# Optimization experiments

Hardware: AMD Instinct MI355X
Metric: run time of the kernel (lower is better)

The kernel has to match this reference:

```python
import jax, jax.numpy as jnp
import numpy as np
from jax import lax

D = 300          # embedding dim (data.x.shape[1])
H = 1024         # hidden_state_dim
H2 = H // 2
V_SENSES = 25000   # last_idx_senses
V_GLOBALS = 50000  # last_idx_globals - last_idx_senses
NUM_NODES = 80000
T = 1024           # seq_len (batch=1)


def _lin_init(k, out_f, in_f):
    # torch.nn.Linear default: U(-1/sqrt(in), 1/sqrt(in)) for W and b
    kw, kb = jax.random.split(k)
    lim = 1.0 / np.sqrt(in_f)
    W = jax.random.uniform(kw, (out_f, in_f), jnp.float32, -lim, lim)
    b = jax.random.uniform(kb, (out_f,), jnp.float32, -lim, lim)
    return W, b


def setup_inputs() -> dict:
    key = jax.random.key(0)
    ks = jax.random.split(key, 6)
    X = jax.random.normal(ks[0], (NUM_NODES, D), jnp.float32) * 0.1
    W1, b1 = _lin_init(ks[1], H, D + H)
    W2, b2 = _lin_init(ks[2], H2, H + H2)
    Wg, bg = _lin_init(ks[3], V_GLOBALS, H2)
    Ws, bs = _lin_init(ks[4], V_SENSES, H2)
    indices = jax.random.randint(ks[5], (1, T), 0, NUM_NODES, jnp.int32)
    return {"X": X, "W1": W1, "b1": b1, "W2": W2, "b2": b2,
            "Wg": Wg, "bg": bg, "Ws": Ws, "bs": bs, "indices": indices}


def reference(X, W1, b1, W2, b2, Wg, bg, Ws, bs, indices):
    # Sequential RNN over flattened (batch, seq) steps; memory_h1/h2 start at
    # zeros and carry across all steps (as the in-place .data.copy_ does).
    # Dropout is treated as identity (eval mode).
    idx = indices.reshape(-1)  # [T]

    def step(carry, i):
        h1, h2 = carry  # [H], [H2]
        e = X[i]  # gather current-word embedding, [D]
        h1n = jax.nn.leaky_relu(
            jnp.dot(W1, jnp.concatenate([e, h1])) + b1, negative_slope=0.01)
        h2n = jax.nn.leaky_relu(
            jnp.dot(W2, jnp.concatenate([h1n, h2])) + b2, negative_slope=0.01)
        return (h1n, h2n), h2n

    init = (jnp.zeros((H,), X.dtype), jnp.zeros((H2,), X.dtype))
    _, h2s = lax.scan(step, init, idx)  # h2s: [T, H2]

    # Output projections batched over all timesteps (same math as per-step).
    logp_globals = jax.nn.log_softmax(h2s @ Wg.T + bg, axis=-1)  # [T, V_GLOBALS]
    logp_senses = jax.nn.log_softmax(h2s @ Ws.T + bs, axis=-1)   # [T, V_SENSES]
    return logp_globals, logp_senses
```

## Files before the change

### kernel.cpp

```cpp
#include <hip/hip_runtime.h>
#include <hip/hip_bf16.h>
#include <stdint.h>

#define T_STEPS 1024
#define NH1 1024
#define NH2 512
#define D_IN 300
#define W1_LD 1324
#define W2_LD 1536
#define NVG 50000
#define NVS 25000

typedef unsigned long long u64;
typedef __bf16 bf16x8 __attribute__((ext_vector_type(8)));
typedef short s16x8 __attribute__((ext_vector_type(8)));
typedef float f32x4 __attribute__((ext_vector_type(4)));

__global__ __launch_bounds__(256) void e_kernel(
    const float* __restrict__ X,
    const float* __restrict__ W1,
    const float* __restrict__ b1,
    const int* __restrict__ idx,
    float* __restrict__ E,
    unsigned* __restrict__ ctl)
{
  if (blockIdx.x == 0 && threadIdx.x < 16) ctl[threadIdx.x] = 0u;

  __shared__ float Xs[32 * 300];
  const int rb = blockIdx.x & 7;
  const int tb = blockIdx.x >> 3;
  const int r0 = rb * 128;
  const int t0 = tb * 32;

  for (int t = 0; t < 32; ++t) {
    int node = idx[t0 + t];
    for (int c = threadIdx.x; c < 300; c += 256)
      Xs[t * 300 + c] = X[(size_t)node * D_IN + c];
  }
  __syncthreads();

  const int rl = threadIdx.x & 127;
  const int th = threadIdx.x >> 7;
  const int tbase = th * 16;
  const int r = r0 + rl;

  float acc[16];
  const float bias = b1[r];
#pragma unroll
  for (int tt = 0; tt < 16; ++tt) acc[tt] = bias;

  const float* wrow = W1 + (size_t)r * W1_LD;
  for (int c0 = 0; c0 < 300; c0 += 4) {
    float w0 = wrow[c0 + 0];
    float w1 = wrow[c0 + 1];
    float w2 = wrow[c0 + 2];
    float w3 = wrow[c0 + 3];
#pragma unroll
    for (int tt = 0; tt < 16; ++tt) {
      const float* xr = Xs + (tbase + tt) * 300 + c0;
      acc[tt] += w0 * xr[0] + w1 * xr[1] + w2 * xr[2] + w3 * xr[3];
    }
  }
#pragma unroll
  for (int tt = 0; tt < 16; ++tt)
    E[(size_t)(t0 + tbase + tt) * NH1 + r] = acc[tt];
}

__global__ __launch_bounds__(256, 2) void rnn_kernel(
    const float* __restrict__ W1,
    const float* __restrict__ W2,
    const float* __restrict__ b2,
    const float* __restrict__ E,
    u64* __restrict__ buf1,
    u64* __restrict__ buf2,
    __hip_bfloat16* __restrict__ h2s,
    unsigned* __restrict__ ctl)
{
  __shared__ float lds1[2][NH1];
  __shared__ float lds2[2][NH2];
  __shared__ int s_role;

  if (threadIdx.x == 0) {
    int xcd;
    asm volatile("s_getreg_b32 %0, hwreg(HW_REG_XCC_ID)" : "=s"(xcd));
    xcd &= 7;
    unsigned rk = atomicAdd(&ctl[xcd], 1u);
    int role = -1;
    if (rk < 64u) {
      if (rk == 63u) atomicCAS(&ctl[8], 0u, (unsigned)(xcd + 1));
      unsigned wnr;
      while ((wnr = __hip_atomic_load(&ctl[8], __ATOMIC_RELAXED,
                                      __HIP_MEMORY_SCOPE_AGENT)) == 0u)
        __builtin_amdgcn_s_sleep(16);
      if (wnr == (unsigned)(xcd + 1)) role = (int)rk;
    }
    s_role = role;
  }
  __syncthreads();
  if (s_role < 0) return;
  const int b = s_role;

  const int lane = threadIdx.x & 63;
  const int w = threadIdx.x >> 6;
  const int wvid = b * 4 + w;
  const int r1 = wvid * 4;
  const int r2 = wvid * 2;
  const int q = (w + b) & 3;

  float w1r[4][16];
#pragma unroll
  for (int i = 0; i < 4; ++i)
#pragma unroll
    for (int j = 0; j < 16; ++j)
      w1r[i][j] = W1[(size_t)(r1 + i) * W1_LD + D_IN + lane + 64 * j];

  float w2r[2][24];
#pragma unroll
  for (int i = 0; i < 2; ++i)
#pragma unroll
    for (int j = 0; j < 24; ++j)
      w2r[i][j] = W2[(size_t)(r2 + i) * W2_LD + lane + 64 * j];

  const float b2a = b2[r2];
  const float b2b = b2[r2 + 1];

  for (int s = 0; s <= T_STEPS; ++s) {
    float ev = 0.f;
    if (s < T_STEPS) ev = E[(size_t)s * NH1 + r1 + (lane & 3)];

    float v1[4] = {0.f, 0.f, 0.f, 0.f};
    float v2[2] = {0.f, 0.f};
    unsigned miss = 0;
    if (s >= 1) miss |= 0xFu;
    if (s >= 2) miss |= 0x30u;
    const u64* p1 = buf1 + (size_t)(s & 3) * NH1 + 256 * q + lane;
    const u64* p2 = buf2 + (size_t)((s - 1) & 3) * NH2 + 128 * q + lane;
    const unsigned tag1 = (unsigned)s;
    const unsigned tag2 = (unsigned)(s - 1);

    while (miss) {
      u64 t1[4], t2[2];
      asm volatile(
          "global_load_dwordx2 %0, %6, off sc0 sc1\n\t"
          "global_load_dwordx2 %1, %6, off offset:512 sc0 sc1\n\t"
          "global_load_dwordx2 %2, %6, off offset:1024 sc0 sc1\n\t"
          "global_load_dwordx2 %3, %6, off offset:1536 sc0 sc1\n\t"
          "global_load_dwordx2 %4, %7, off sc0 sc1\n\t"
          "global_load_dwordx2 %5, %7, off offset:512 sc0 sc1\n\t"
          "s_waitcnt vmcnt(0)"
          : "=&v"(t1[0]), "=&v"(t1[1]), "=&v"(t1[2]), "=&v"(t1[3]),
            "=&v"(t2[0]), "=&v"(t2[1])
          : "v"(p1), "v"(p2)
          : "memory");
#pragma unroll
      for (int j = 0; j < 4; ++j)
        if ((miss & (1u << j)) && (unsigned)(t1[j] >> 32) == tag1) {
          v1[j] = __uint_as_float((unsigned)t1[j]);
          miss &= ~(1u << j);
        }
#pragma unroll
      for (int j = 0; j < 2; ++j)
        if ((miss & (0x10u << j)) && (unsigned)(t2[j] >> 32) == tag2) {
          v2[j] = __uint_as_float((unsigned)t2[j]);
          miss &= ~(0x10u << j);
        }
    }

    const int pb = s & 1;
#pragma unroll
    for (int j = 0; j < 4; ++j) lds1[pb][256 * q + 64 * j + lane] = v1[j];
#pragma unroll
    for (int j = 0; j < 2; ++j) lds2[pb][128 * q + 64 * j + lane] = v2[j];
    __syncthreads();

    float a0 = 0.f, a1 = 0.f, a2 = 0.f, a3 = 0.f, a4 = 0.f, a5 = 0.f;
#pragma unroll
    for (int j = 0; j < 16; ++j) {
      float h = lds1[pb][lane + 64 * j];
      a0 += w1r[0][j] * h;
      a1 += w1r[1][j] * h;
      a2 += w1r[2][j] * h;
      a3 += w1r[3][j] * h;
      a4 += w2r[0][j] * h;
      a5 += w2r[1][j] * h;
    }
#pragma unroll
    for (int j = 0; j < 8; ++j) {
      float h = lds2[pb][lane + 64 * j];
      a4 += w2r[0][16 + j] * h;
      a5 += w2r[1][16 + j] * h;
    }

#pragma unroll
    for (int off = 32; off; off >>= 1) {
      a0 += __shfl_xor(a0, off);
      a1 += __shfl_xor(a1, off);
      a2 += __shfl_xor(a2, off);
      a3 += __shfl_xor(a3, off);
    }
    if (s < T_STEPS && lane < 4) {
      float x = (lane == 0 ? a0 : lane == 1 ? a1 : lane == 2 ? a2 : a3) + ev;
      float h = x > 0.f ? x : 0.01f * x;
      u64 pk = ((u64)(unsigned)(s + 1) << 32) | (u64)__float_as_uint(h);
      u64* dst = buf1 + (size_t)((s + 1) & 3) * NH1 + r1 + lane;
      asm volatile("global_store_dwordx2 %0, %1, off sc0"
                   :: "v"(dst), "v"(pk) : "memory");
    }

    if (s >= 1) {
#pragma unroll
      for (int off = 32; off; off >>= 1) {
        a4 += __shfl_xor(a4, off);
        a5 += __shfl_xor(a5, off);
      }
      if (lane >= 4 && lane < 6) {
        int i = lane - 4;
        float x = (i == 0 ? a4 : a5) + (i == 0 ? b2a : b2b);
        float h = x > 0.f ? x : 0.01f * x;
        u64 pk = ((u64)(unsigned)s << 32) | (u64)__float_as_uint(h);
        u64* dst = buf2 + (size_t)(s & 3) * NH2 + r2 + i;
        asm volatile("global_store_dwordx2 %0, %1, off sc0"
                     :: "v"(dst), "v"(pk) : "memory");
        h2s[(size_t)(s - 1) * NH2 + r2 + i] = __float2bfloat16(h);
      }
    }
  }
}

__global__ __launch_bounds__(256, 1) void gemm_kernel(
    const __hip_bfloat16* __restrict__ A,
    const float* __restrict__ B,
    const float* __restrict__ bias,
    float* __restrict__ C,
    int N)
{
  __shared__ short As[256 * 64];
  __shared__ short Bs[128 * 64];
  const int tid = threadIdx.x;
  const int lane = tid & 63;
  const int wv = tid >> 6;
  const int wm = (wv & 1) * 128;
  const int wn = (wv >> 1) * 64;
  const int m0 = blockIdx.x * 256;
  const int n0 = blockIdx.y * 128;
  const int ml = lane & 15;
  const int kq = lane >> 4;

  f32x4 acc[8][4];
#pragma unroll
  for (int i = 0; i < 8; ++i)
#pragma unroll
    for (int j = 0; j < 4; ++j)
      acc[i][j] = (f32x4){0.f, 0.f, 0.f, 0.f};

  for (int kb = 0; kb < 512; kb += 64) {
    __syncthreads();
#pragma unroll
    for (int q = 0; q < 8; ++q) {
      int ch = q * 256 + tid;
      int row = ch >> 3;
      int kc = ch & 7;
      int phys = kc ^ (row & 7);
      s16x8 av = *(const s16x8*)((const short*)A + (size_t)(m0 + row) * 512 + kb + kc * 8);
      *(s16x8*)(As + row * 64 + phys * 8) = av;
    }
#pragma unroll
    for (int q = 0; q < 4; ++q) {
      int ch = q * 256 + tid;
      int row = ch >> 3;
      int kc = ch & 7;
      int phys = kc ^ (row & 7);
      int gr = n0 + row;
      if (gr >= N) gr = N - 1;
      const float* src = B + (size_t)gr * 512 + kb + kc * 8;
      f32x4 f0 = *(const f32x4*)(src);
      f32x4 f1 = *(const f32x4*)(src + 4);
      bf16x8 bv;
      bv[0] = (__bf16)f0[0]; bv[1] = (__bf16)f0[1];
      bv[2] = (__bf16)f0[2]; bv[3] = (__bf16)f0[3];
      bv[4] = (__bf16)f1[0]; bv[5] = (__bf16)f1[1];
      bv[6] = (__bf16)f1[2]; bv[7] = (__bf16)f1[3];
      *(bf16x8*)(Bs + row * 64 + phys * 8) = bv;
    }
    __syncthreads();
#pragma unroll
    for (int ks = 0; ks < 2; ++ks) {
      bf16x8 af[8], bfr[4];
#pragma unroll
      for (int i = 0; i < 8; ++i) {
        int row = wm + 16 * i + ml;
        int phys = (ks * 4 + kq) ^ (row & 7);
        af[i] = *(const bf16x8*)(As + row * 64 + phys * 8);
      }
#pragma unroll
      for (int j = 0; j < 4; ++j) {
        int row = wn + 16 * j + ml;
        int phys = (ks * 4 + kq) ^ (row & 7);
        bfr[j] = *(const bf16x8*)(Bs + row * 64 + phys * 8);
      }
#pragma unroll
      for (int i = 0; i < 8; ++i)
#pragma unroll
        for (int j = 0; j < 4; ++j)
          acc[i][j] = __builtin_amdgcn_mfma_f32_16x16x32_bf16(af[i], bfr[j], acc[i][j], 0, 0, 0);
    }
  }

  float bv[4];
#pragma unroll
  for (int j = 0; j < 4; ++j) {
    int n = n0 + wn + 16 * j + ml;
    bv[j] = (n < N) ? bias[n] : 0.f;
  }
#pragma unroll
  for (int i = 0; i < 8; ++i) {
    int mrow = m0 + wm + 16 * i + kq * 4;
#pragma unroll
    for (int j = 0; j < 4; ++j) {
      int n = n0 + wn + 16 * j + ml;
      if (n < N) {
#pragma unroll
        for (int r = 0; r < 4; ++r)
          C[(size_t)(mrow + r) * N + n] = acc[i][j][r] + bv[j];
      }
    }
  }
}

__global__ __launch_bounds__(256) void norm_kernel(float* __restrict__ out)
{
  const int b = blockIdx.x;
  const int t = b & 1023;
  const int seg = b >> 10;
  const size_t base = seg == 0 ? (size_t)t * NVG
                               : (size_t)1024 * NVG + (size_t)t * NVS;
  const int len = seg == 0 ? NVG : NVS;
  float* p = out + base;
  const int lane = threadIdx.x & 63;
  const int wv = threadIdx.x >> 6;
  __shared__ float red[4];

  float m = -3.0e38f;
  for (int i = threadIdx.x; i < len; i += 256)
    m = fmaxf(m, p[i]);
#pragma unroll
  for (int off = 32; off; off >>= 1) m = fmaxf(m, __shfl_xor(m, off));
  if (lane == 0) red[wv] = m;
  __syncthreads();
  m = fmaxf(fmaxf(red[0], red[1]), fmaxf(red[2], red[3]));
  __syncthreads();

  float sum = 0.f;
  for (int i = threadIdx.x; i < len; i += 256)
    sum += expf(p[i] - m);
#pragma unroll
  for (int off = 32; off; off >>= 1) sum += __shfl_xor(sum, off);
  if (lane == 0) red[wv] = sum;
  __syncthreads();
  sum = red[0] + red[1] + red[2] + red[3];
  const float lse = m + logf(sum);

  for (int i = threadIdx.x; i < len; i += 256)
    p[i] = p[i] - lse;
}

extern "C" void kernel_launch(void* const* d_in, const int* in_sizes, int n_in,
                              void* d_out, int out_size, void* d_ws, size_t ws_size,
                              hipStream_t stream) {
  const float* X  = (const float*)d_in[0];
  const float* W1 = (const float*)d_in[1];
  const float* b1 = (const float*)d_in[2];
  const float* W2 = (const float*)d_in[3];
  const float* b2 = (const float*)d_in[4];
  const float* Wg = (const float*)d_in[5];
  const float* bg = (const float*)d_in[6];
  const float* Ws = (const float*)d_in[7];
  const float* bs = (const float*)d_in[8];
  const int* idx = (const int*)d_in[9];
  float* out = (float*)d_out;

  char* ws = (char*)d_ws;
  float* E = (float*)ws;
  __hip_bfloat16* h2s = (__hip_bfloat16*)(ws + (size_t)4194304);
  u64* buf1 = (u64*)(ws + (size_t)5242880);
  u64* buf2 = (u64*)(ws + (size_t)5275648);
  unsigned* ctl = (unsigned*)(out + (size_t)1024 * (NVG + NVS) - 16);

  e_kernel<<<256, 256, 0, stream>>>(X, W1, b1, idx, E, ctl);
  rnn_kernel<<<512, 256, 0, stream>>>(W1, W2, b2, E, buf1, buf2, h2s, ctl);
  gemm_kernel<<<dim3(4, 391), 256, 0, stream>>>(h2s, Wg, bg, out, NVG);
  gemm_kernel<<<dim3(4, 196), 256, 0, stream>>>(h2s, Ws, bs,
                                                out + (size_t)1024 * NVG, NVS);
  norm_kernel<<<2048, 256, 0, stream>>>(out);
}
```

Measured before the change: 3.178 ms.

## Split recurrent step into two phases so layer-1 output publishes before waiting on h2

Each step of the persistent RNN kernel used to poll for h1(s) and h2(s-1) together, then compute both layers. It now polls only h1(s), computes and publishes the layer-1 result first, and only then polls h2(s-1) and computes layer 2. The aim is to shorten the critical path of the cross-block layer-1 recurrence, so it no longer waits on the slower h2 flags. In exchange it adds a second __syncthreads and a second polling loop per step, and lds1 is read twice.

```diff
diff --git a/kernel.cpp b/kernel.cpp
--- a/kernel.cpp
+++ b/kernel.cpp
@@ -127,53 +127,37 @@
   for (int s = 0; s <= T_STEPS; ++s) {
     float ev = 0.f;
     if (s < T_STEPS) ev = E[(size_t)s * NH1 + r1 + (lane & 3)];
+    const int pb = s & 1;
 
     float v1[4] = {0.f, 0.f, 0.f, 0.f};
-    float v2[2] = {0.f, 0.f};
-    unsigned miss = 0;
-    if (s >= 1) miss |= 0xFu;
-    if (s >= 2) miss |= 0x30u;
+    unsigned missA = (s >= 1) ? 0xFu : 0u;
     const u64* p1 = buf1 + (size_t)(s & 3) * NH1 + 256 * q + lane;
-    const u64* p2 = buf2 + (size_t)((s - 1) & 3) * NH2 + 128 * q + lane;
     const unsigned tag1 = (unsigned)s;
-    const unsigned tag2 = (unsigned)(s - 1);
-
-    while (miss) {
-      u64 t1[4], t2[2];
+
+    while (missA) {
+      u64 t1[4];
       asm volatile(
-          "global_load_dwordx2 %0, %6, off sc0 sc1\n\t"
-          "global_load_dwordx2 %1, %6, off offset:512 sc0 sc1\n\t"
-          "global_load_dwordx2 %2, %6, off offset:1024 sc0 sc1\n\t"
-          "global_load_dwordx2 %3, %6, off offset:1536 sc0 sc1\n\t"
-          "global_load_dwordx2 %4, %7, off sc0 sc1\n\t"
-          "global_load_dwordx2 %5, %7, off offset:512 sc0 sc1\n\t"
+          "global_load_dwordx2 %0, %4, off sc0 sc1\n\t"
+          "global_load_dwordx2 %1, %4, off offset:512 sc0 sc1\n\t"
+          "global_load_dwordx2 %2, %4, off offset:1024 sc0 sc1\n\t"
+          "global_load_dwordx2 %3, %4, off offset:1536 sc0 sc1\n\t"
           "s_waitcnt vmcnt(0)"
-          : "=&v"(t1[0]), "=&v"(t1[1]), "=&v"(t1[2]), "=&v"(t1[3]),
-            "=&v"(t2[0]), "=&v"(t2[1])
-          : "v"(p1), "v"(p2)
+          : "=&v"(t1[0]), "=&v"(t1[1]), "=&v"(t1[2]), "=&v"(t1[3])
+          : "v"(p1)
           : "memory");
 #pragma unroll
       for (int j = 0; j < 4; ++j)
-        if ((miss & (1u << j)) && (unsigned)(t1[j] >> 32) == tag1) {
+        if ((missA & (1u << j)) && (unsigned)(t1[j] >> 32) == tag1) {
           v1[j] = __uint_as_float((unsigned)t1[j]);
-          miss &= ~(1u << j);
+          missA &= ~(1u << j);
         }
-#pragma unroll
-      for (int j = 0; j < 2; ++j)
-        if ((miss & (0x10u << j)) && (unsigned)(t2[j] >> 32) == tag2) {
-          v2[j] = __uint_as_float((unsigned)t2[j]);
-          miss &= ~(0x10u << j);
-        }
-    }
-
-    const int pb = s & 1;
+    }
+
 #pragma unroll
     for (int j = 0; j < 4; ++j) lds1[pb][256 * q + 64 * j + lane] = v1[j];
-#pragma unroll
-    for (int j = 0; j < 2; ++j) lds2[pb][128 * q + 64 * j + lane] = v2[j];
     __syncthreads();
 
-    float a0 = 0.f, a1 = 0.f, a2 = 0.f, a3 = 0.f, a4 = 0.f, a5 = 0.f;
+    float a0 = 0.f, a1 = 0.f, a2 = 0.f, a3 = 0.f;
 #pragma unroll
     for (int j = 0; j < 16; ++j) {
       float h = lds1[pb][lane + 64 * j];
@@ -181,16 +165,7 @@
       a1 += w1r[1][j] * h;
       a2 += w1r[2][j] * h;
       a3 += w1r[3][j] * h;
-      a4 += w2r[0][j] * h;
-      a5 += w2r[1][j] * h;
-    }
-#pragma unroll
-    for (int j = 0; j < 8; ++j) {
-      float h = lds2[pb][lane + 64 * j];
-      a4 += w2r[0][16 + j] * h;
-      a5 += w2r[1][16 + j] * h;
-    }
-
+    }
 #pragma unroll
     for (int off = 32; off; off >>= 1) {
       a0 += __shfl_xor(a0, off);
@@ -207,7 +182,46 @@
                    :: "v"(dst), "v"(pk) : "memory");
     }
 
+    float v2[2] = {0.f, 0.f};
+    unsigned missB = (s >= 2) ? 0x3u : 0u;
+    const u64* p2 = buf2 + (size_t)((s - 1) & 3) * NH2 + 128 * q + lane;
+    const unsigned tag2 = (unsigned)(s - 1);
+
+    while (missB) {
+      u64 t2[2];
+      asm volatile(
+          "global_load_dwordx2 %0, %2, off sc0 sc1\n\t"
+          "global_load_dwordx2 %1, %2, off offset:512 sc0 sc1\n\t"
+          "s_waitcnt vmcnt(0)"
+          : "=&v"(t2[0]), "=&v"(t2[1])
+          : "v"(p2)
+          : "memory");
+#pragma unroll
+      for (int j = 0; j < 2; ++j)
+        if ((missB & (1u << j)) && (unsigned)(t2[j] >> 32) == tag2) {
+          v2[j] = __uint_as_float((unsigned)t2[j]);
+          missB &= ~(1u << j);
+        }
+    }
+
+#pragma unroll
+    for (int j = 0; j < 2; ++j) lds2[pb][128 * q + 64 * j + lane] = v2[j];
+    __syncthreads();
+
     if (s >= 1) {
+      float a4 = 0.f, a5 = 0.f;
+#pragma unroll
+      for (int j = 0; j < 16; ++j) {
+        float h = lds1[pb][lane + 64 * j];
+        a4 += w2r[0][j] * h;
+        a5 += w2r[1][j] * h;
+      }
+#pragma unroll
+      for (int j = 0; j < 8; ++j) {
+        float h = lds2[pb][lane + 64 * j];
+        a4 += w2r[0][16 + j] * h;
+        a5 += w2r[1][16 + j] * h;
+      }
 #pragma unroll
       for (int off = 32; off; off >>= 1) {
         a4 += __shfl_xor(a4, off);
```

After: 3.331 ms. 1.05x slower.

## Use 512-thread RNN blocks on 32 CUs to halve the polling load per wave

Applied to the files above, without the earlier changes.

The persistent RNN kernel now uses 32 blocks of 8 waves on one XCD instead of 64 blocks of 4 waves. Each wave polls and loads only an eighth of the shared hidden-state buffers rather than a quarter, which cuts per-wave global polling traffic and the number of participating blocks in the cross-block handoff. The cost is a heavier __syncthreads across 8 waves and more waves sharing each CU's register file and issue slots.

```diff
diff --git a/kernel.cpp b/kernel.cpp
--- a/kernel.cpp
+++ b/kernel.cpp
@@ -66,7 +66,7 @@
     E[(size_t)(t0 + tbase + tt) * NH1 + r] = acc[tt];
 }
 
-__global__ __launch_bounds__(256, 2) void rnn_kernel(
+__global__ __launch_bounds__(512, 2) void rnn_kernel(
     const float* __restrict__ W1,
     const float* __restrict__ W2,
     const float* __restrict__ b2,
@@ -86,8 +86,8 @@
     xcd &= 7;
     unsigned rk = atomicAdd(&ctl[xcd], 1u);
     int role = -1;
-    if (rk < 64u) {
-      if (rk == 63u) atomicCAS(&ctl[8], 0u, (unsigned)(xcd + 1));
+    if (rk < 32u) {
+      if (rk == 31u) atomicCAS(&ctl[8], 0u, (unsigned)(xcd + 1));
       unsigned wnr;
       while ((wnr = __hip_atomic_load(&ctl[8], __ATOMIC_RELAXED,
                                       __HIP_MEMORY_SCOPE_AGENT)) == 0u)
@@ -102,10 +102,10 @@
 
   const int lane = threadIdx.x & 63;
   const int w = threadIdx.x >> 6;
-  const int wvid = b * 4 + w;
+  const int wvid = b * 8 + w;
   const int r1 = wvid * 4;
   const int r2 = wvid * 2;
-  const int q = (w + b) & 3;
+  const int oct = (w + b) & 7;
 
   float w1r[4][16];
 #pragma unroll
@@ -128,49 +128,42 @@
     float ev = 0.f;
     if (s < T_STEPS) ev = E[(size_t)s * NH1 + r1 + (lane & 3)];
 
-    float v1[4] = {0.f, 0.f, 0.f, 0.f};
-    float v2[2] = {0.f, 0.f};
+    float v1[2] = {0.f, 0.f};
+    float v2 = 0.f;
     unsigned miss = 0;
-    if (s >= 1) miss |= 0xFu;
-    if (s >= 2) miss |= 0x30u;
-    const u64* p1 = buf1 + (size_t)(s & 3) * NH1 + 256 * q + lane;
-    const u64* p2 = buf2 + (size_t)((s - 1) & 3) * NH2 + 128 * q + lane;
+    if (s >= 1) miss |= 0x3u;
+    if (s >= 2) miss |= 0x4u;
+    const u64* p1 = buf1 + (size_t)(s & 3) * NH1 + 128 * oct + lane;
+    const u64* p2 = buf2 + (size_t)((s - 1) & 3) * NH2 + 64 * oct + lane;
     const unsigned tag1 = (unsigned)s;
     const unsigned tag2 = (unsigned)(s - 1);
 
     while (miss) {
-      u64 t1[4], t2[2];
+      u64 t1[2], t2;
       asm volatile(
-          "global_load_dwordx2 %0, %6, off sc0 sc1\n\t"
-          "global_load_dwordx2 %1, %6, off offset:512 sc0 sc1\n\t"
-          "global_load_dwordx2 %2, %6, off offset:1024 sc0 sc1\n\t"
-          "global_load_dwordx2 %3, %6, off offset:1536 sc0 sc1\n\t"
-          "global_load_dwordx2 %4, %7, off sc0 sc1\n\t"
-          "global_load_dwordx2 %5, %7, off offset:512 sc0 sc1\n\t"
+          "global_load_dwordx2 %0, %3, off sc0 sc1\n\t"
+          "global_load_dwordx2 %1, %3, off offset:512 sc0 sc1\n\t"
+          "global_load_dwordx2 %2, %4, off sc0 sc1\n\t"
           "s_waitcnt vmcnt(0)"
-          : "=&v"(t1[0]), "=&v"(t1[1]), "=&v"(t1[2]), "=&v"(t1[3]),
-            "=&v"(t2[0]), "=&v"(t2[1])
+          : "=&v"(t1[0]), "=&v"(t1[1]), "=&v"(t2)
           : "v"(p1), "v"(p2)
           : "memory");
 #pragma unroll
-      for (int j = 0; j < 4; ++j)
+      for (int j = 0; j < 2; ++j)
         if ((miss & (1u << j)) && (unsigned)(t1[j] >> 32) == tag1) {
           v1[j] = __uint_as_float((unsigned)t1[j]);
           miss &= ~(1u << j);
         }
-#pragma unroll
-      for (int j = 0; j < 2; ++j)
-        if ((miss & (0x10u << j)) && (unsigned)(t2[j] >> 32) == tag2) {
-          v2[j] = __uint_as_float((unsigned)t2[j]);
-          miss &= ~(0x10u << j);
-        }
+      if ((miss & 0x4u) && (unsigned)(t2 >> 32) == tag2) {
+        v2 = __uint_as_float((unsigned)t2);
+        miss &= ~0x4u;
+      }
     }
 
     const int pb = s & 1;
 #pragma unroll
-    for (int j = 0; j < 4; ++j) lds1[pb][256 * q + 64 * j + lane] = v1[j];
-#pragma unroll
-    for (int j = 0; j < 2; ++j) lds2[pb][128 * q + 64 * j + lane] = v2[j];
+    for (int j = 0; j < 2; ++j) lds1[pb][128 * oct + 64 * j + lane] = v1[j];
+    lds2[pb][64 * oct + lane] = v2;
     __syncthreads();
 
     float a0 = 0.f, a1 = 0.f, a2 = 0.f, a3 = 0.f, a4 = 0.f, a5 = 0.f;
@@ -387,7 +380,7 @@
   unsigned* ctl = (unsigned*)(out + (size_t)1024 * (NVG + NVS) - 16);
 
   e_kernel<<<256, 256, 0, stream>>>(X, W1, b1, idx, E, ctl);
-  rnn_kernel<<<512, 256, 0, stream>>>(W1, W2, b2, E, buf1, buf2, h2s, ctl);
+  rnn_kernel<<<256, 512, 0, stream>>>(W1, W2, b2, E, buf1, buf2, h2s, ctl);
   gemm_kernel<<<dim3(4, 391), 256, 0, stream>>>(h2s, Wg, bg, out, NVG);
   gemm_kernel<<<dim3(4, 196), 256, 0, stream>>>(h2s, Ws, bs,
                                                 out + (size_t)1024 * NVG, NVS);
```

Result: faster. 2.966 ms (-6.7%).
